# Optimization experiments

Hardware: AMD Instinct MI355X
Metric: run time of the kernel (lower is better)

The kernel has to match this reference:

```python
import jax, jax.numpy as jnp
import numpy as np

B, C, F, T = 64, 1, 1024, 512
CF = C * F
D = 128  # fc1 output / LSTM sequence length
H = 1    # LSTM hidden size (out_channel=1)


def setup_inputs() -> dict:
    key = jax.random.key(0)
    ks = jax.random.split(key, 20)
    n = lambda k, shp, s=0.1: jax.random.normal(k, shp, dtype=jnp.float32) * s
    return {
        "x": jax.random.normal(ks[0], (B, C, F, T), dtype=jnp.float32),
        "fc1_w": n(ks[1], (D, CF), 0.03), "fc1_b": n(ks[2], (D,)),
        # PyTorch LSTM gate order: i, f, g, o; weights (4H, I) and (4H, H)
        "wih_f": n(ks[3], (4 * H, 1)), "whh_f": n(ks[4], (4 * H, H)),
        "bih_f": n(ks[5], (4 * H,)), "bhh_f": n(ks[6], (4 * H,)),
        "wih_b": n(ks[7], (4 * H, 1)), "whh_b": n(ks[8], (4 * H, H)),
        "bih_b": n(ks[9], (4 * H,)), "bhh_b": n(ks[10], (4 * H,)),
        "lout_w": n(ks[11], (1, 2 * H)), "lout_b": n(ks[12], (1,)),
        "emb_w1": n(ks[13], (D, D)), "emb_b1": n(ks[14], (D,)),
        "emb_w2": n(ks[15], (D, D)), "emb_b2": n(ks[16], (D,)),
    }


def _lstm(xs, wih, whh, bih, bhh):
    # xs: (N, S, I) -> (N, S, H). Gate order i,f,g,o as in torch.
    N = xs.shape[0]
    Hh = whh.shape[1]
    b = bih + bhh

    def step(carry, xt):
        h, c = carry
        gates = xt @ wih.T + h @ whh.T + b  # (N, 4H)
        i, f, g, o = jnp.split(gates, 4, axis=-1)
        c = jax.nn.sigmoid(f) * c + jax.nn.sigmoid(i) * jnp.tanh(g)
        h = jax.nn.sigmoid(o) * jnp.tanh(c)
        return (h, c), h

    h0 = jnp.zeros((N, Hh), xs.dtype)
    _, hs = jax.lax.scan(step, (h0, h0), jnp.swapaxes(xs, 0, 1))
    return jnp.swapaxes(hs, 0, 1)  # (N, S, H)


def reference(x, fc1_w, fc1_b, wih_f, whh_f, bih_f, bhh_f,
              wih_b, whh_b, bih_b, bhh_b, lout_w, lout_b,
              emb_w1, emb_b1, emb_w2, emb_b2):
    Bb, Cc, Ff, Tt = x.shape
    # Merge the time loop into the batch dim: every timestep uses the same weights.
    xt = jnp.moveaxis(x, 3, 1).reshape(Bb * Tt, Cc * Ff)        # (B*T, CF)
    h = xt @ fc1_w.T + fc1_b                                     # (B*T, 128)
    seq = h[:, :, None]                                          # (B*T, 128, 1): seq len 128, feat 1
    fwd = _lstm(seq, wih_f, whh_f, bih_f, bhh_f)                 # (B*T, 128, H)
    bwd = _lstm(seq[:, ::-1], wih_b, whh_b, bih_b, bhh_b)[:, ::-1]
    hcat = jnp.concatenate([fwd, bwd], axis=-1)                  # (B*T, 128, 2H)
    y = (hcat @ lout_w.T + lout_b)[..., 0]                       # (B*T, 128)
    e = y @ emb_w1.T + emb_b1
    e = jnp.where(e >= 0, e, 0.2 * e)                            # LeakyReLU(0.2)
    e = e @ emb_w2.T + emb_b2                                    # (B*T, 128)
    emb_time = e.reshape(Bb, Tt, D)                              # stacked over time
    return jnp.mean(emb_time, axis=1)                            # mean_linear: (B, 128)
```

## Files before the change

### kernel.cpp

```cpp
#include <hip/hip_runtime.h>
#include <hip/hip_bf16.h>

typedef __attribute__((ext_vector_type(8))) short short8;
typedef __attribute__((ext_vector_type(4))) float f32x4;

#define TDIM 512
#define FDIM 1024

__device__ __forceinline__ float sigm(float x)  { return 1.0f / (1.0f + __expf(-x)); }
__device__ __forceinline__ float tanh_f(float x){ return 1.0f - 2.0f / (__expf(2.0f * x) + 1.0f); }

__global__ __launch_bounds__(256) void prep_k(const float* __restrict__ w1,
                                              const float* __restrict__ w2,
                                              const float* __restrict__ fc1_w,
                                              float* __restrict__ w1t,
                                              float* __restrict__ w2t,
                                              ushort* __restrict__ wb16) {
    int blk = blockIdx.x;
    int tid = threadIdx.x;
    if (blk < 128) {
        int idx = blk * 256 + tid;
        int sel = idx >> 14;
        int within = idx & 16383;
        int k = within >> 7, d = within & 127;
        if (sel == 0) w1t[within] = w1[d * 128 + k];
        else          w2t[within] = w2[d * 128 + k];
    } else {
        int idx = (blk - 128) * 256 + tid;
        float4 v = reinterpret_cast<const float4*>(fc1_w)[idx];
        ushort4 o;
        o.x = __bfloat16_as_ushort(__float2bfloat16(v.x));
        o.y = __bfloat16_as_ushort(__float2bfloat16(v.y));
        o.z = __bfloat16_as_ushort(__float2bfloat16(v.z));
        o.w = __bfloat16_as_ushort(__float2bfloat16(v.w));
        reinterpret_cast<ushort4*>(wb16)[idx] = o;
    }
}

__global__ __launch_bounds__(256, 4) void fused_k(
    const float* __restrict__ x,
    const ushort* __restrict__ wb16, const float* __restrict__ fc1_b,
    const float* __restrict__ wih_f, const float* __restrict__ whh_f,
    const float* __restrict__ bih_f, const float* __restrict__ bhh_f,
    const float* __restrict__ wih_b, const float* __restrict__ whh_b,
    const float* __restrict__ bih_b, const float* __restrict__ bhh_b,
    const float* __restrict__ lout_w, const float* __restrict__ lout_b,
    const float* __restrict__ w1t, const float* __restrict__ emb_b1,
    float* __restrict__ partials)
{
    __shared__ float h_lds[32 * 128];
    __shared__ float y[32 * 128];

    int tid = threadIdx.x;
    int blk = blockIdx.x;
    int b  = blk >> 4;
    int t0 = (blk & 15) * 32;

    int lane = tid & 63;
    int wid  = tid >> 6;
    int wr = wid >> 1, wc = wid & 1;
    int l15 = lane & 15, g = lane >> 4;

    const float*  xl = x + (size_t)b * (FDIM * TDIM) + (t0 + wr * 16 + l15);
    const ushort* wl = wb16 + (size_t)(wc * 64 + l15) * FDIM + g * 8;

    f32x4 acc[4] = {f32x4{0,0,0,0}, f32x4{0,0,0,0}, f32x4{0,0,0,0}, f32x4{0,0,0,0}};

#pragma unroll 2
    for (int k0 = 0; k0 < FDIM; k0 += 32) {
        float av[8];
#pragma unroll
        for (int j = 0; j < 8; ++j)
            av[j] = xl[(size_t)(k0 + g * 8 + j) * TDIM];
        short8 a;
#pragma unroll
        for (int j = 0; j < 8; ++j)
            a[j] = (short)__bfloat16_as_ushort(__float2bfloat16(av[j]));
#pragma unroll
        for (int ni = 0; ni < 4; ++ni) {
            short8 bfr = *reinterpret_cast<const short8*>(wl + k0 + ni * 16 * FDIM);
            acc[ni] = __builtin_amdgcn_mfma_f32_16x16x32_bf16(a, bfr, acc[ni], 0, 0, 0);
        }
    }

#pragma unroll
    for (int ni = 0; ni < 4; ++ni) {
        int col = wc * 64 + ni * 16 + l15;
        float bias = fc1_b[col];
#pragma unroll
        for (int r = 0; r < 4; ++r) {
            int row = wr * 16 + g * 4 + r;
            h_lds[row * 128 + (col ^ ((row & 7) << 2))] = acc[ni][r] + bias;
        }
    }

    float lb = lout_b[0];
    for (int i = tid; i < 32 * 128; i += 256) y[i] = lb;
    __syncthreads();

    if (tid < 64) {
        int row = tid >> 1, dir = tid & 1;
        int sw = (row & 7) << 2;
        const float* wih = dir ? wih_b : wih_f;
        const float* whh = dir ? whh_b : whh_f;
        const float* bi  = dir ? bih_b : bih_f;
        const float* bh  = dir ? bhh_b : bhh_f;
        float wi0 = wih[0], wi1 = wih[1], wi2 = wih[2], wi3 = wih[3];
        float wh0 = whh[0], wh1 = whh[1], wh2 = whh[2], wh3 = whh[3];
        float c0 = bi[0] + bh[0], c1 = bi[1] + bh[1], c2 = bi[2] + bh[2], c3 = bi[3] + bh[3];
        float wsel = lout_w[dir];
        float hh = 0.f, cc = 0.f;
        for (int s = 0; s < 128; ++s) {
            int d = dir ? (127 - s) : s;
            float xv = h_lds[row * 128 + (d ^ sw)];
            float gi = fmaf(wi0, xv, fmaf(wh0, hh, c0));
            float gf = fmaf(wi1, xv, fmaf(wh1, hh, c1));
            float gg = fmaf(wi2, xv, fmaf(wh2, hh, c2));
            float go = fmaf(wi3, xv, fmaf(wh3, hh, c3));
            cc = sigm(gf) * cc + sigm(gi) * tanh_f(gg);
            hh = sigm(go) * tanh_f(cc);
            y[row * 128 + (d ^ sw)] += wsel * hh;
        }
    }
    __syncthreads();

    int d1 = tid & 127;
    int half = tid >> 7;
    int r0 = half * 16;
    float accv[16];
#pragma unroll
    for (int j = 0; j < 16; ++j) accv[j] = 0.f;
    for (int k4 = 0; k4 < 128; k4 += 4) {
        float w0v = w1t[(k4 + 0) * 128 + d1];
        float w1v = w1t[(k4 + 1) * 128 + d1];
        float w2v = w1t[(k4 + 2) * 128 + d1];
        float w3v = w1t[(k4 + 3) * 128 + d1];
#pragma unroll
        for (int j = 0; j < 16; ++j) {
            int r = r0 + j;
            int sw = (r & 7) << 2;
            float4 yv = *reinterpret_cast<const float4*>(&y[r * 128 + (k4 ^ sw)]);
            accv[j] = fmaf(yv.x, w0v, accv[j]);
            accv[j] = fmaf(yv.y, w1v, accv[j]);
            accv[j] = fmaf(yv.z, w2v, accv[j]);
            accv[j] = fmaf(yv.w, w3v, accv[j]);
        }
    }
    float b1e = emb_b1[d1];
    float ssum = 0.f;
#pragma unroll
    for (int j = 0; j < 16; ++j) {
        float e = accv[j] + b1e;
        ssum += (e >= 0.f) ? e : 0.2f * e;
    }
    h_lds[half * 128 + d1] = ssum;
    __syncthreads();
    if (tid < 128)
        partials[(size_t)blk * 128 + tid] = h_lds[tid] + h_lds[128 + tid];
}

__global__ __launch_bounds__(128) void final_k(const float* __restrict__ partials,
                                               const float* __restrict__ w2t,
                                               const float* __restrict__ emb_b2,
                                               float* __restrict__ out) {
    __shared__ float S[128];
    int b = blockIdx.x, tid = threadIdx.x;
    float s = 0.f;
#pragma unroll
    for (int p = 0; p < 16; ++p) s += partials[(size_t)(b * 16 + p) * 128 + tid];
    S[tid] = s * (1.0f / 512.0f);
    __syncthreads();
    float acc = emb_b2[tid];
    for (int k = 0; k < 128; ++k) acc = fmaf(S[k], w2t[k * 128 + tid], acc);
    out[b * 128 + tid] = acc;
}

extern "C" void kernel_launch(void* const* d_in, const int* in_sizes, int n_in,
                              void* d_out, int out_size, void* d_ws, size_t ws_size,
                              hipStream_t stream) {
    const float* x      = (const float*)d_in[0];
    const float* fc1_w  = (const float*)d_in[1];
    const float* fc1_b  = (const float*)d_in[2];
    const float* wih_f  = (const float*)d_in[3];
    const float* whh_f  = (const float*)d_in[4];
    const float* bih_f  = (const float*)d_in[5];
    const float* bhh_f  = (const float*)d_in[6];
    const float* wih_b  = (const float*)d_in[7];
    const float* whh_b  = (const float*)d_in[8];
    const float* bih_b  = (const float*)d_in[9];
    const float* bhh_b  = (const float*)d_in[10];
    const float* lout_w = (const float*)d_in[11];
    const float* lout_b = (const float*)d_in[12];
    const float* emb_w1 = (const float*)d_in[13];
    const float* emb_b1 = (const float*)d_in[14];
    const float* emb_w2 = (const float*)d_in[15];
    const float* emb_b2 = (const float*)d_in[16];
    float* out = (float*)d_out;

    float* partials = (float*)d_ws;
    float* w1t  = partials + 1024 * 128;
    float* w2t  = w1t + 16384;
    ushort* wb16 = (ushort*)(w2t + 16384);

    prep_k<<<256, 256, 0, stream>>>(emb_w1, emb_w2, fc1_w, w1t, w2t, wb16);
    fused_k<<<1024, 256, 0, stream>>>(x, wb16, fc1_b,
                                      wih_f, whh_f, bih_f, bhh_f,
                                      wih_b, whh_b, bih_b, bhh_b,
                                      lout_w, lout_b, w1t, emb_b1, partials);
    final_k<<<64, 128, 0, stream>>>(partials, w2t, emb_b2, out);
}
```

Before: 322.8 us.

## Use bf16 LDS buffers, MFMA for embedding layer, and software-pipeline fc1 loads

```diff
diff --git a/kernel.cpp b/kernel.cpp
--- a/kernel.cpp
+++ b/kernel.cpp
@@ -9,31 +9,31 @@
 
 __device__ __forceinline__ float sigm(float x)  { return 1.0f / (1.0f + __expf(-x)); }
 __device__ __forceinline__ float tanh_f(float x){ return 1.0f - 2.0f / (__expf(2.0f * x) + 1.0f); }
-
-__global__ __launch_bounds__(256) void prep_k(const float* __restrict__ w1,
+__device__ __forceinline__ float  bf2f(ushort u) { return __uint_as_float(((unsigned)u) << 16); }
+__device__ __forceinline__ ushort f2bf(float f)  { return __bfloat16_as_ushort(__float2bfloat16(f)); }
+__device__ __forceinline__ int hidx(int row, int d) { return row * 128 + (d ^ ((row & 7) << 3)); }
+
+__global__ __launch_bounds__(256) void prep_k(const float* __restrict__ fc1_w,
+                                              const float* __restrict__ w1,
                                               const float* __restrict__ w2,
-                                              const float* __restrict__ fc1_w,
-                                              float* __restrict__ w1t,
-                                              float* __restrict__ w2t,
-                                              ushort* __restrict__ wb16) {
-    int blk = blockIdx.x;
-    int tid = threadIdx.x;
+                                              ushort* __restrict__ wb16,
+                                              ushort* __restrict__ w1b,
+                                              float* __restrict__ w2t) {
+    int blk = blockIdx.x, tid = threadIdx.x;
     if (blk < 128) {
         int idx = blk * 256 + tid;
-        int sel = idx >> 14;
-        int within = idx & 16383;
-        int k = within >> 7, d = within & 127;
-        if (sel == 0) w1t[within] = w1[d * 128 + k];
-        else          w2t[within] = w2[d * 128 + k];
+        float4 v = reinterpret_cast<const float4*>(fc1_w)[idx];
+        ushort4 o = { f2bf(v.x), f2bf(v.y), f2bf(v.z), f2bf(v.w) };
+        reinterpret_cast<ushort4*>(wb16)[idx] = o;
+    } else if (blk < 144) {
+        int idx = (blk - 128) * 256 + tid;
+        float4 v = reinterpret_cast<const float4*>(w1)[idx];
+        ushort4 o = { f2bf(v.x), f2bf(v.y), f2bf(v.z), f2bf(v.w) };
+        reinterpret_cast<ushort4*>(w1b)[idx] = o;
     } else {
-        int idx = (blk - 128) * 256 + tid;
-        float4 v = reinterpret_cast<const float4*>(fc1_w)[idx];
-        ushort4 o;
-        o.x = __bfloat16_as_ushort(__float2bfloat16(v.x));
-        o.y = __bfloat16_as_ushort(__float2bfloat16(v.y));
-        o.z = __bfloat16_as_ushort(__float2bfloat16(v.z));
-        o.w = __bfloat16_as_ushort(__float2bfloat16(v.w));
-        reinterpret_cast<ushort4*>(wb16)[idx] = o;
+        int idx = (blk - 144) * 256 + tid;
+        int k = idx >> 7, d = idx & 127;
+        w2t[idx] = w2[d * 128 + k];
     }
 }
 
@@ -45,11 +45,11 @@
     const float* __restrict__ wih_b, const float* __restrict__ whh_b,
     const float* __restrict__ bih_b, const float* __restrict__ bhh_b,
     const float* __restrict__ lout_w, const float* __restrict__ lout_b,
-    const float* __restrict__ w1t, const float* __restrict__ emb_b1,
+    const ushort* __restrict__ w1b, const float* __restrict__ emb_b1,
     float* __restrict__ partials)
 {
-    __shared__ float h_lds[32 * 128];
-    __shared__ float y[32 * 128];
+    __shared__ __align__(16) ushort h16[32 * 128];
+    __shared__ __align__(16) ushort y16[32 * 128];
 
     int tid = threadIdx.x;
     int blk = blockIdx.x;
@@ -64,23 +64,35 @@
     const float*  xl = x + (size_t)b * (FDIM * TDIM) + (t0 + wr * 16 + l15);
     const ushort* wl = wb16 + (size_t)(wc * 64 + l15) * FDIM + g * 8;
 
+    float  av[2][8];
+    short8 bq[2][4];
+#pragma unroll
+    for (int j = 0; j < 8; ++j) av[0][j] = xl[(size_t)(g * 8 + j) * TDIM];
+#pragma unroll
+    for (int j = 0; j < 8; ++j) av[1][j] = xl[(size_t)(32 + g * 8 + j) * TDIM];
+#pragma unroll
+    for (int ni = 0; ni < 4; ++ni)
+        bq[0][ni] = *reinterpret_cast<const short8*>(wl + (size_t)ni * 16 * FDIM);
+
     f32x4 acc[4] = {f32x4{0,0,0,0}, f32x4{0,0,0,0}, f32x4{0,0,0,0}, f32x4{0,0,0,0}};
 
-#pragma unroll 2
-    for (int k0 = 0; k0 < FDIM; k0 += 32) {
-        float av[8];
+    for (int it = 0; it < 32; ++it) {
+        int k0 = it * 32;
+        int cur = it & 1;
+        short8 a;
+#pragma unroll
+        for (int j = 0; j < 8; ++j) a[j] = (short)f2bf(av[cur][j]);
+        int kpfA = (k0 + 64) & 1023;
 #pragma unroll
         for (int j = 0; j < 8; ++j)
-            av[j] = xl[(size_t)(k0 + g * 8 + j) * TDIM];
-        short8 a;
-#pragma unroll
-        for (int j = 0; j < 8; ++j)
-            a[j] = (short)__bfloat16_as_ushort(__float2bfloat16(av[j]));
-#pragma unroll
-        for (int ni = 0; ni < 4; ++ni) {
-            short8 bfr = *reinterpret_cast<const short8*>(wl + k0 + ni * 16 * FDIM);
-            acc[ni] = __builtin_amdgcn_mfma_f32_16x16x32_bf16(a, bfr, acc[ni], 0, 0, 0);
-        }
+            av[cur][j] = xl[(size_t)(kpfA + g * 8 + j) * TDIM];
+        int kpfB = (k0 + 32) & 1023;
+#pragma unroll
+        for (int ni = 0; ni < 4; ++ni)
+            bq[cur ^ 1][ni] = *reinterpret_cast<const short8*>(wl + kpfB + (size_t)ni * 16 * FDIM);
+#pragma unroll
+        for (int ni = 0; ni < 4; ++ni)
+            acc[ni] = __builtin_amdgcn_mfma_f32_16x16x32_bf16(a, bq[cur][ni], acc[ni], 0, 0, 0);
     }
 
 #pragma unroll
@@ -90,17 +102,21 @@
 #pragma unroll
         for (int r = 0; r < 4; ++r) {
             int row = wr * 16 + g * 4 + r;
-            h_lds[row * 128 + (col ^ ((row & 7) << 2))] = acc[ni][r] + bias;
-        }
-    }
-
-    float lb = lout_b[0];
-    for (int i = tid; i < 32 * 128; i += 256) y[i] = lb;
+            h16[hidx(row, col)] = f2bf(acc[ni][r] + bias);
+        }
+    }
+
+    {
+        ushort lbu = f2bf(lout_b[0]);
+        ushort4 lv = { lbu, lbu, lbu, lbu };
+#pragma unroll
+        for (int i = 0; i < 4; ++i)
+            reinterpret_cast<ushort4*>(y16)[i * 256 + tid] = lv;
+    }
     __syncthreads();
 
     if (tid < 64) {
         int row = tid >> 1, dir = tid & 1;
-        int sw = (row & 7) << 2;
         const float* wih = dir ? wih_b : wih_f;
         const float* whh = dir ? whh_b : whh_f;
         const float* bi  = dir ? bih_b : bih_f;
@@ -112,51 +128,54 @@
         float hh = 0.f, cc = 0.f;
         for (int s = 0; s < 128; ++s) {
             int d = dir ? (127 - s) : s;
-            float xv = h_lds[row * 128 + (d ^ sw)];
+            float xv = bf2f(h16[hidx(row, d)]);
             float gi = fmaf(wi0, xv, fmaf(wh0, hh, c0));
             float gf = fmaf(wi1, xv, fmaf(wh1, hh, c1));
             float gg = fmaf(wi2, xv, fmaf(wh2, hh, c2));
             float go = fmaf(wi3, xv, fmaf(wh3, hh, c3));
             cc = sigm(gf) * cc + sigm(gi) * tanh_f(gg);
             hh = sigm(go) * tanh_f(cc);
-            y[row * 128 + (d ^ sw)] += wsel * hh;
-        }
-    }
-    __syncthreads();
-
-    int d1 = tid & 127;
-    int half = tid >> 7;
-    int r0 = half * 16;
-    float accv[16];
-#pragma unroll
-    for (int j = 0; j < 16; ++j) accv[j] = 0.f;
-    for (int k4 = 0; k4 < 128; k4 += 4) {
-        float w0v = w1t[(k4 + 0) * 128 + d1];
-        float w1v = w1t[(k4 + 1) * 128 + d1];
-        float w2v = w1t[(k4 + 2) * 128 + d1];
-        float w3v = w1t[(k4 + 3) * 128 + d1];
-#pragma unroll
-        for (int j = 0; j < 16; ++j) {
-            int r = r0 + j;
-            int sw = (r & 7) << 2;
-            float4 yv = *reinterpret_cast<const float4*>(&y[r * 128 + (k4 ^ sw)]);
-            accv[j] = fmaf(yv.x, w0v, accv[j]);
-            accv[j] = fmaf(yv.y, w1v, accv[j]);
-            accv[j] = fmaf(yv.z, w2v, accv[j]);
-            accv[j] = fmaf(yv.w, w3v, accv[j]);
-        }
-    }
-    float b1e = emb_b1[d1];
-    float ssum = 0.f;
-#pragma unroll
-    for (int j = 0; j < 16; ++j) {
-        float e = accv[j] + b1e;
-        ssum += (e >= 0.f) ? e : 0.2f * e;
-    }
-    h_lds[half * 128 + d1] = ssum;
-    __syncthreads();
-    if (tid < 128)
-        partials[(size_t)blk * 128 + tid] = h_lds[tid] + h_lds[128 + tid];
+            int yi = hidx(row, d);
+            y16[yi] = f2bf(bf2f(y16[yi]) + wsel * hh);
+        }
+    }
+    __syncthreads();
+
+    f32x4 accE[4] = {f32x4{0,0,0,0}, f32x4{0,0,0,0}, f32x4{0,0,0,0}, f32x4{0,0,0,0}};
+    {
+        int ro = wr * 16 + l15;
+        int sw = (ro & 7) << 3;
+        const ushort* w1p = w1b + (size_t)(wc * 64 + l15) * 128 + g * 8;
+#pragma unroll
+        for (int k0 = 0; k0 < 128; k0 += 32) {
+            short8 ya = *reinterpret_cast<const short8*>(&y16[ro * 128 + ((k0 + g * 8) ^ sw)]);
+#pragma unroll
+            for (int ni = 0; ni < 4; ++ni) {
+                short8 wf = *reinterpret_cast<const short8*>(w1p + k0 + (size_t)ni * 16 * 128);
+                accE[ni] = __builtin_amdgcn_mfma_f32_16x16x32_bf16(ya, wf, accE[ni], 0, 0, 0);
+            }
+        }
+    }
+    float* psum = reinterpret_cast<float*>(h16);
+#pragma unroll
+    for (int ni = 0; ni < 4; ++ni) {
+        int d1 = wc * 64 + ni * 16 + l15;
+        float b1v = emb_b1[d1];
+        float s = 0.f;
+#pragma unroll
+        for (int j = 0; j < 4; ++j) {
+            float e = accE[ni][j] + b1v;
+            s += (e >= 0.f) ? e : 0.2f * e;
+        }
+        psum[(wr * 4 + g) * 128 + d1] = s;
+    }
+    __syncthreads();
+    if (tid < 128) {
+        float s = 0.f;
+#pragma unroll
+        for (int rg = 0; rg < 8; ++rg) s += psum[rg * 128 + tid];
+        partials[(size_t)blk * 128 + tid] = s;
+    }
 }
 
 __global__ __launch_bounds__(128) void final_k(const float* __restrict__ partials,
@@ -197,15 +216,15 @@
     const float* emb_b2 = (const float*)d_in[16];
     float* out = (float*)d_out;
 
-    float* partials = (float*)d_ws;
-    float* w1t  = partials + 1024 * 128;
-    float* w2t  = w1t + 16384;
+    float*  partials = (float*)d_ws;
+    float*  w2t  = partials + 1024 * 128;
     ushort* wb16 = (ushort*)(w2t + 16384);
-
-    prep_k<<<256, 256, 0, stream>>>(emb_w1, emb_w2, fc1_w, w1t, w2t, wb16);
+    ushort* w1b  = wb16 + 131072;
+
+    prep_k<<<208, 256, 0, stream>>>(fc1_w, emb_w1, emb_w2, wb16, w1b, w2t);
     fused_k<<<1024, 256, 0, stream>>>(x, wb16, fc1_b,
                                       wih_f, whh_f, bih_f, bhh_f,
                                       wih_b, whh_b, bih_b, bhh_b,
-                                      lout_w, lout_b, w1t, emb_b1, partials);
+                                      lout_w, lout_b, w1b, emb_b1, partials);
     final_k<<<64, 128, 0, stream>>>(partials, w2t, emb_b2, out);
 }
```

Measured after the change: 528.2 us. 1.64x slower.
